# Kernel tuning notes

Measured on AMD Instinct MI355X. Metric: run time of the kernel, lower is better.

The kernel has to match this reference:

```python
import jax, jax.numpy as jnp
import numpy as np

N_CAR, N_LIGHT, N_STOP = 180000, 10000, 10000
N = N_CAR + N_LIGHT + N_STOP
E = 6_400_000

# LossConfig defaults
LAMBDA_RECON, LAMBDA_RULE, LAMBDA_ATTN, LAMBDA_REG = 1.0, 0.5, 0.3, 1e-4
W_ATTN_GAT, W_ATTN_RULE = 0.5, 0.5
VIOL_THRESH = 0.5


def setup_inputs() -> dict:
    key = jax.random.key(0)
    ks = jax.random.split(key, 8)
    eps = 1e-6
    model_scores = jnp.clip(jax.random.uniform(ks[0], (N_CAR,), jnp.float32), eps, 1.0 - eps)
    rule_scores = jnp.clip(jax.random.uniform(ks[1], (N_CAR,), jnp.float32), eps, 1.0 - eps)
    alpha_gat = jax.random.uniform(ks[2], (E,), jnp.float32)
    beta_rule = jax.random.uniform(ks[3], (N_CAR,), jnp.float32)
    src = jax.random.randint(ks[4], (E,), 0, N)
    dst = jax.random.randint(ks[5], (E,), 0, N)
    edge_index = jnp.stack([src, dst], axis=0)
    # cars first (type 0), then lights (1), then stop lines (2)
    entity_types = jnp.concatenate([
        jnp.zeros((N_CAR,), jnp.int32),
        jnp.ones((N_LIGHT,), jnp.int32),
        jnp.full((N_STOP,), 2, jnp.int32),
    ])
    param0 = jax.random.normal(ks[6], (4096, 4096), jnp.float32) * 0.02
    param1 = jax.random.normal(ks[7], (4096, 4096), jnp.float32) * 0.02
    return {
        "model_scores": model_scores, "rule_scores": rule_scores,
        "alpha_gat": alpha_gat, "beta_rule": beta_rule,
        "edge_index": edge_index, "entity_types": entity_types,
        "param0": param0, "param1": param1,
    }


def _bce(x, t):
    # torch F.binary_cross_entropy clamps log at -100
    log_x = jnp.clip(jnp.log(x), -100.0)
    log_1mx = jnp.clip(jnp.log1p(-x), -100.0)
    return jnp.mean(-(t * log_x + (1.0 - t) * log_1mx))


def _gat_attn_loss(alpha_gat, edge_index, entity_types, violation_mask):
    src, dst = edge_index[0], edge_index[1]
    dst_t = entity_types[dst]
    rule_edge = (dst_t == 1) | (dst_t == 2)
    masked = jnp.where(rule_edge, alpha_gat, -jnp.inf)
    # fused segment-max over source nodes replaces the per-car Python loop
    seg_max = jax.ops.segment_max(masked, src, num_segments=N)  # [N]
    car_ids = jnp.nonzero(entity_types == 0, size=N_CAR)[0]      # [N_car]
    max_attn = seg_max[car_ids]                                  # [N_car]
    valid = jnp.isfinite(max_attn) & violation_mask             # cars w/ rule neighbor
    safe = jnp.where(valid, max_attn, 0.0)
    total = jnp.sum(jnp.where(valid, (1.0 - safe) ** 2, 0.0))
    cnt = jnp.sum(valid)
    return jnp.where(cnt > 0, total / jnp.maximum(cnt, 1).astype(total.dtype), 0.0)


def _rule_attn_loss(beta_rule, violation_mask):
    total = jnp.sum(jnp.where(violation_mask, (1.0 - beta_rule) ** 2, 0.0))
    cnt = jnp.sum(violation_mask)
    return jnp.where(cnt > 0, total / jnp.maximum(cnt, 1).astype(total.dtype), 0.0)


@jax.jit
def reference(model_scores, rule_scores, alpha_gat, beta_rule, edge_index, entity_types, param0, param1):
    L_recon = _bce(model_scores, rule_scores)
    L_rule = jnp.mean((model_scores - rule_scores) ** 2)
    violation_mask = rule_scores > VIOL_THRESH
    any_viol = jnp.any(violation_mask)
    L_attn_gat = jnp.where(any_viol, _gat_attn_loss(alpha_gat, edge_index, entity_types, violation_mask), 0.0)
    L_attn_rule = jnp.where(any_viol, _rule_attn_loss(beta_rule, violation_mask), 0.0)
    L_attn = W_ATTN_GAT * L_attn_gat + W_ATTN_RULE * L_attn_rule
    L_reg = jnp.sum(param0 ** 2) + jnp.sum(param1 ** 2)
    L_total = (LAMBDA_RECON * L_recon + LAMBDA_RULE * L_rule
               + LAMBDA_ATTN * L_attn + LAMBDA_REG * L_reg)
    num_violations = jnp.sum(violation_mask).astype(jnp.float32)
    return (L_total, L_recon, L_rule, L_attn, L_attn_gat, L_attn_rule, L_reg, num_violations)
```

## Files before the change

kernel.cpp:

```cpp
#include <hip/hip_runtime.h>

#define N_CAR   180000
#define NE      6400000
#define P_ELEMS (4096 * 4096)
#define P4      (P_ELEMS / 4)

#define WORK_BLOCKS  4096
#define WORK_T       (WORK_BLOCKS * 256)
#define REG_ITERS    (P4 / WORK_T)
#define EDGE_QUADS   (NE / 4)

#define CAR_BLOCKS   ((N_CAR + 255) / 256)
#define MASK_WORDS   5632
#define MASK_QUADS   (MASK_WORDS / 4)
#define MASK_BLOCKS  704
#define NCOPY        8

typedef float    f4 __attribute__((ext_vector_type(4)));
typedef int      i4 __attribute__((ext_vector_type(4)));
typedef unsigned u32;


__device__ __forceinline__ float wave_reduce_sum(float s) {
#pragma unroll
    for (int off = 32; off > 0; off >>= 1) s += __shfl_down(s, off, 64);
    return s;
}

__global__ void __launch_bounds__(256) mask_kernel(const float* __restrict__ rs,
                                                   u32* __restrict__ mask) {
    int j = blockIdx.x * 256 + threadIdx.x;
    int bit = (j < N_CAR) && (rs[j] > 0.5f);
    unsigned long long b = __ballot(bit);
    if ((threadIdx.x & 63) == 0) {
        int w = (j >> 6) * 2;
        mask[w]     = (u32)(b);
        mask[w + 1] = (u32)(b >> 32);
    }
}

template <int NC, int SCOPE>
__global__ void __launch_bounds__(256) work_kernel(const i4* __restrict__ src4,
                                                   const i4* __restrict__ dst4,
                                                   const f4* __restrict__ alpha4,
                                                   int* __restrict__ segmax,
                                                   const u32* __restrict__ maskg,
                                                   const f4* __restrict__ p0,
                                                   const f4* __restrict__ p1,
                                                   float* __restrict__ regpart) {
    __shared__ u32 smask[MASK_WORDS];
    __shared__ float red[4];
    int t = blockIdx.x * 256 + threadIdx.x;

    {
        const i4* m4 = (const i4*)maskg;
        i4* s4 = (i4*)smask;
        for (int q = threadIdx.x; q < MASK_QUADS; q += 256) s4[q] = m4[q];
    }

    int base = 0;
    if (NC > 1) {
        int xcd = (int)(__builtin_amdgcn_s_getreg((31u << 11) | 20) & (NC - 1));
        base = xcd * N_CAR;
    }
    __syncthreads();

    for (int q = t; q < EDGE_QUADS; q += WORK_T) {
        i4 d  = __builtin_nontemporal_load(&dst4[q]);
        i4 sv = __builtin_nontemporal_load(&src4[q]);
        f4 al = __builtin_nontemporal_load(&alpha4[q]);
#define EDGE_DO(C)                                                              \
        if (d.C >= N_CAR && sv.C < N_CAR &&                                     \
            ((smask[sv.C >> 5] >> (sv.C & 31)) & 1u)) {                         \
            __hip_atomic_fetch_max(&segmax[base + sv.C], __float_as_int(al.C),  \
                                   __ATOMIC_RELAXED, SCOPE);                    \
        }
        EDGE_DO(x)
        EDGE_DO(y)
        EDGE_DO(z)
        EDGE_DO(w)
#undef EDGE_DO
    }

    f4 a = {0.f, 0.f, 0.f, 0.f};
#pragma unroll
    for (int k = 0; k < REG_ITERS; ++k) {
        f4 v = __builtin_nontemporal_load(&p0[t + k * WORK_T]);
        a += v * v;
    }
#pragma unroll
    for (int k = 0; k < REG_ITERS; ++k) {
        f4 v = __builtin_nontemporal_load(&p1[t + k * WORK_T]);
        a += v * v;
    }
    float s = (a.x + a.y) + (a.z + a.w);
    s = wave_reduce_sum(s);
    int wave = threadIdx.x >> 6;
    int lane = threadIdx.x & 63;
    if (lane == 0) red[wave] = s;
    __syncthreads();
    if (threadIdx.x == 0)
        regpart[blockIdx.x] = red[0] + red[1] + red[2] + red[3];
}

template <int NC>
__global__ void __launch_bounds__(256) car_kernel(const float* __restrict__ ms,
                                                  const float* __restrict__ rs,
                                                  const float* __restrict__ beta,
                                                  const int* __restrict__ segmax,
                                                  float* __restrict__ carpart) {
    int i = blockIdx.x * blockDim.x + threadIdx.x;
    float vals[6] = {0.f, 0.f, 0.f, 0.f, 0.f, 0.f};
    if (i < N_CAR) {
        float x = ms[i];
        float t = rs[i];
        float lx  = fmaxf(logf(x), -100.0f);
        float l1x = fmaxf(log1pf(-x), -100.0f);
        vals[0] = -(t * lx + (1.0f - t) * l1x);
        float df = x - t;
        vals[1] = df * df;
        if (t > 0.5f) {
            vals[2] = 1.0f;
            float b = beta[i];
            vals[3] = (1.0f - b) * (1.0f - b);
            int mi = segmax[i];
#pragma unroll
            for (int c = 1; c < NC; ++c)
                mi = max(mi, segmax[c * N_CAR + i]);
            if (mi >= 0) {
                float m = __int_as_float(mi);
                vals[4] = (1.0f - m) * (1.0f - m);
                vals[5] = 1.0f;
            }
        }
    }
    __shared__ float red[4][6];
    int wave = threadIdx.x >> 6;
    int lane = threadIdx.x & 63;
#pragma unroll
    for (int k = 0; k < 6; ++k) {
        float s = wave_reduce_sum(vals[k]);
        if (lane == 0) red[wave][k] = s;
    }
    __syncthreads();
    if (threadIdx.x == 0) {
#pragma unroll
        for (int k = 0; k < 6; ++k)
            carpart[blockIdx.x * 6 + k] = red[0][k] + red[1][k] + red[2][k] + red[3][k];
    }
}

__global__ void __launch_bounds__(256) finalize_kernel(const float* __restrict__ regpart,
                                                       const float* __restrict__ carpart,
                                                       float* __restrict__ out) {
    int tid = threadIdx.x;
    float rsum = 0.0f;
    for (int i = tid; i < WORK_BLOCKS; i += 256) rsum += regpart[i];
    float c[6] = {0.f, 0.f, 0.f, 0.f, 0.f, 0.f};
    for (int r = tid; r < CAR_BLOCKS; r += 256) {
#pragma unroll
        for (int k = 0; k < 6; ++k) c[k] += carpart[r * 6 + k];
    }
    __shared__ float red[4][7];
    int wave = tid >> 6;
    int lane = tid & 63;
    {
        float s = wave_reduce_sum(rsum);
        if (lane == 0) red[wave][6] = s;
    }
#pragma unroll
    for (int k = 0; k < 6; ++k) {
        float s = wave_reduce_sum(c[k]);
        if (lane == 0) red[wave][k] = s;
    }
    __syncthreads();
    if (tid == 0) {
        float tot[7];
#pragma unroll
        for (int k = 0; k < 7; ++k)
            tot[k] = red[0][k] + red[1][k] + red[2][k] + red[3][k];
        const float inv_ncar = 1.0f / (float)N_CAR;
        float L_recon = tot[0] * inv_ncar;
        float L_rule  = tot[1] * inv_ncar;
        float vc      = tot[2];
        float L_attn_rule = (vc > 0.0f) ? tot[3] / vc : 0.0f;
        float gat_cnt = tot[5];
        float L_attn_gat = (vc > 0.0f && gat_cnt > 0.0f) ? tot[4] / gat_cnt : 0.0f;
        float L_attn = 0.5f * L_attn_gat + 0.5f * L_attn_rule;
        float L_reg  = tot[6];
        float L_total = 1.0f * L_recon + 0.5f * L_rule + 0.3f * L_attn + 1e-4f * L_reg;
        out[0] = L_total;
        out[1] = L_recon;
        out[2] = L_rule;
        out[3] = L_attn;
        out[4] = L_attn_gat;
        out[5] = L_attn_rule;
        out[6] = L_reg;
        out[7] = vc;
    }
}

extern "C" void kernel_launch(void* const* d_in, const int* in_sizes, int n_in,
                              void* d_out, int out_size, void* d_ws, size_t ws_size,
                              hipStream_t stream) {
    const float* model_scores = (const float*)d_in[0];
    const float* rule_scores  = (const float*)d_in[1];
    const float* alpha_gat    = (const float*)d_in[2];
    const float* beta_rule    = (const float*)d_in[3];
    const int*   edge_index   = (const int*)d_in[4];
    const float* param0       = (const float*)d_in[6];
    const float* param1       = (const float*)d_in[7];
    float* out = (float*)d_out;

    const int* src = edge_index;
    const int* dst = edge_index + NE;

    const size_t seg_bytes8 = (size_t)NCOPY * N_CAR * sizeof(int);
    const size_t tail_bytes = (size_t)(MASK_WORDS + WORK_BLOCKS + CAR_BLOCKS * 6) * 4;

    if (ws_size >= seg_bytes8 + tail_bytes) {
        int* segmax  = (int*)d_ws;
        u32* mask    = (u32*)((char*)d_ws + seg_bytes8);
        float* regpart = (float*)(mask + MASK_WORDS);
        float* carpart = regpart + WORK_BLOCKS;

        mask_kernel<<<MASK_BLOCKS, 256, 0, stream>>>(rule_scores, mask);
        work_kernel<NCOPY, __HIP_MEMORY_SCOPE_WORKGROUP>
            <<<WORK_BLOCKS, 256, 0, stream>>>(
                (const i4*)src, (const i4*)dst, (const f4*)alpha_gat, segmax,
                mask, (const f4*)param0, (const f4*)param1, regpart);
        car_kernel<NCOPY><<<CAR_BLOCKS, 256, 0, stream>>>(
            model_scores, rule_scores, beta_rule, segmax, carpart);
        finalize_kernel<<<1, 256, 0, stream>>>(regpart, carpart, out);
    } else {
        int* segmax  = (int*)d_ws;
        u32* mask    = (u32*)((char*)d_ws + (size_t)N_CAR * sizeof(int));
        float* regpart = (float*)(mask + MASK_WORDS);
        float* carpart = regpart + WORK_BLOCKS;

        mask_kernel<<<MASK_BLOCKS, 256, 0, stream>>>(rule_scores, mask);
        work_kernel<1, __HIP_MEMORY_SCOPE_AGENT>
            <<<WORK_BLOCKS, 256, 0, stream>>>(
                (const i4*)src, (const i4*)dst, (const f4*)alpha_gat, segmax,
                mask, (const f4*)param0, (const f4*)param1, regpart);
        car_kernel<1><<<CAR_BLOCKS, 256, 0, stream>>>(
            model_scores, rule_scores, beta_rule, segmax, carpart);
        finalize_kernel<<<1, 256, 0, stream>>>(regpart, carpart, out);
    }
}
```

Baseline: 218.1 us.

## Drop violation-mask kernel and issue all edge and param loads upfront

Removes the separate mask kernel and the shared-memory violation-mask filter, so edges whose source is any car now perform the atomic max. The violation mask is presumably applied later in car_kernel. The edge loop is fully unrolled into two fixed quads per thread, and all parameter loads are issued before the atomics so memory latency overlaps. It also drops the nontemporal hints. In exchange, about twice as many atomics run, and the many live f4 registers may lower occupancy.

```diff
diff --git a/kernel.cpp b/kernel.cpp
--- a/kernel.cpp
+++ b/kernel.cpp
@@ -11,32 +11,16 @@
 #define EDGE_QUADS   (NE / 4)
 
 #define CAR_BLOCKS   ((N_CAR + 255) / 256)
-#define MASK_WORDS   5632
-#define MASK_QUADS   (MASK_WORDS / 4)
-#define MASK_BLOCKS  704
 #define NCOPY        8
 
 typedef float    f4 __attribute__((ext_vector_type(4)));
 typedef int      i4 __attribute__((ext_vector_type(4)));
-typedef unsigned u32;
 
 
 __device__ __forceinline__ float wave_reduce_sum(float s) {
 #pragma unroll
     for (int off = 32; off > 0; off >>= 1) s += __shfl_down(s, off, 64);
     return s;
-}
-
-__global__ void __launch_bounds__(256) mask_kernel(const float* __restrict__ rs,
-                                                   u32* __restrict__ mask) {
-    int j = blockIdx.x * 256 + threadIdx.x;
-    int bit = (j < N_CAR) && (rs[j] > 0.5f);
-    unsigned long long b = __ballot(bit);
-    if ((threadIdx.x & 63) == 0) {
-        int w = (j >> 6) * 2;
-        mask[w]     = (u32)(b);
-        mask[w + 1] = (u32)(b >> 32);
-    }
 }
 
 template <int NC, int SCOPE>
@@ -44,57 +28,53 @@
                                                    const i4* __restrict__ dst4,
                                                    const f4* __restrict__ alpha4,
                                                    int* __restrict__ segmax,
-                                                   const u32* __restrict__ maskg,
                                                    const f4* __restrict__ p0,
                                                    const f4* __restrict__ p1,
                                                    float* __restrict__ regpart) {
-    __shared__ u32 smask[MASK_WORDS];
-    __shared__ float red[4];
     int t = blockIdx.x * 256 + threadIdx.x;
-
-    {
-        const i4* m4 = (const i4*)maskg;
-        i4* s4 = (i4*)smask;
-        for (int q = threadIdx.x; q < MASK_QUADS; q += 256) s4[q] = m4[q];
-    }
 
     int base = 0;
     if (NC > 1) {
         int xcd = (int)(__builtin_amdgcn_s_getreg((31u << 11) | 20) & (NC - 1));
         base = xcd * N_CAR;
     }
-    __syncthreads();
-
-    for (int q = t; q < EDGE_QUADS; q += WORK_T) {
-        i4 d  = __builtin_nontemporal_load(&dst4[q]);
-        i4 sv = __builtin_nontemporal_load(&src4[q]);
-        f4 al = __builtin_nontemporal_load(&alpha4[q]);
-#define EDGE_DO(C)                                                              \
-        if (d.C >= N_CAR && sv.C < N_CAR &&                                     \
-            ((smask[sv.C >> 5] >> (sv.C & 31)) & 1u)) {                         \
-            __hip_atomic_fetch_max(&segmax[base + sv.C], __float_as_int(al.C),  \
-                                   __ATOMIC_RELAXED, SCOPE);                    \
-        }
-        EDGE_DO(x)
-        EDGE_DO(y)
-        EDGE_DO(z)
-        EDGE_DO(w)
+
+    const bool has2 = (t + WORK_T) < EDGE_QUADS;
+    const int  q1   = has2 ? (t + WORK_T) : t;
+    i4 d0 = dst4[t];
+    i4 s0 = src4[t];
+    f4 a0 = alpha4[t];
+    i4 d1 = dst4[q1];
+    i4 s1 = src4[q1];
+    f4 a1 = alpha4[q1];
+
+    f4 v[2 * REG_ITERS];
+#pragma unroll
+    for (int k = 0; k < REG_ITERS; ++k) v[k] = p0[t + k * WORK_T];
+#pragma unroll
+    for (int k = 0; k < REG_ITERS; ++k) v[REG_ITERS + k] = p1[t + k * WORK_T];
+
+#define EDGE_DO(d, sv, al, C, live)                                             \
+    if ((live) && (d).C >= N_CAR && (sv).C < N_CAR) {                           \
+        __hip_atomic_fetch_max(&segmax[base + (sv).C], __float_as_int((al).C),  \
+                               __ATOMIC_RELAXED, SCOPE);                        \
+    }
+    EDGE_DO(d0, s0, a0, x, true)
+    EDGE_DO(d0, s0, a0, y, true)
+    EDGE_DO(d0, s0, a0, z, true)
+    EDGE_DO(d0, s0, a0, w, true)
+    EDGE_DO(d1, s1, a1, x, has2)
+    EDGE_DO(d1, s1, a1, y, has2)
+    EDGE_DO(d1, s1, a1, z, has2)
+    EDGE_DO(d1, s1, a1, w, has2)
 #undef EDGE_DO
-    }
-
-    f4 a = {0.f, 0.f, 0.f, 0.f};
-#pragma unroll
-    for (int k = 0; k < REG_ITERS; ++k) {
-        f4 v = __builtin_nontemporal_load(&p0[t + k * WORK_T]);
-        a += v * v;
-    }
-#pragma unroll
-    for (int k = 0; k < REG_ITERS; ++k) {
-        f4 v = __builtin_nontemporal_load(&p1[t + k * WORK_T]);
-        a += v * v;
-    }
+
+    f4 a = v[0] * v[0];
+#pragma unroll
+    for (int k = 1; k < 2 * REG_ITERS; ++k) a += v[k] * v[k];
     float s = (a.x + a.y) + (a.z + a.w);
     s = wave_reduce_sum(s);
+    __shared__ float red[4];
     int wave = threadIdx.x >> 6;
     int lane = threadIdx.x & 63;
     if (lane == 0) red[wave] = s;
@@ -216,33 +196,29 @@
     const int* dst = edge_index + NE;
 
     const size_t seg_bytes8 = (size_t)NCOPY * N_CAR * sizeof(int);
-    const size_t tail_bytes = (size_t)(MASK_WORDS + WORK_BLOCKS + CAR_BLOCKS * 6) * 4;
+    const size_t tail_bytes = (size_t)(WORK_BLOCKS + CAR_BLOCKS * 6) * 4;
 
     if (ws_size >= seg_bytes8 + tail_bytes) {
         int* segmax  = (int*)d_ws;
-        u32* mask    = (u32*)((char*)d_ws + seg_bytes8);
-        float* regpart = (float*)(mask + MASK_WORDS);
+        float* regpart = (float*)((char*)d_ws + seg_bytes8);
         float* carpart = regpart + WORK_BLOCKS;
 
-        mask_kernel<<<MASK_BLOCKS, 256, 0, stream>>>(rule_scores, mask);
         work_kernel<NCOPY, __HIP_MEMORY_SCOPE_WORKGROUP>
             <<<WORK_BLOCKS, 256, 0, stream>>>(
                 (const i4*)src, (const i4*)dst, (const f4*)alpha_gat, segmax,
-                mask, (const f4*)param0, (const f4*)param1, regpart);
+                (const f4*)param0, (const f4*)param1, regpart);
         car_kernel<NCOPY><<<CAR_BLOCKS, 256, 0, stream>>>(
             model_scores, rule_scores, beta_rule, segmax, carpart);
         finalize_kernel<<<1, 256, 0, stream>>>(regpart, carpart, out);
     } else {
         int* segmax  = (int*)d_ws;
-        u32* mask    = (u32*)((char*)d_ws + (size_t)N_CAR * sizeof(int));
-        float* regpart = (float*)(mask + MASK_WORDS);
+        float* regpart = (float*)((char*)d_ws + (size_t)N_CAR * sizeof(int));
         float* carpart = regpart + WORK_BLOCKS;
 
-        mask_kernel<<<MASK_BLOCKS, 256, 0, stream>>>(rule_scores, mask);
         work_kernel<1, __HIP_MEMORY_SCOPE_AGENT>
             <<<WORK_BLOCKS, 256, 0, stream>>>(
                 (const i4*)src, (const i4*)dst, (const f4*)alpha_gat, segmax,
-                mask, (const f4*)param0, (const f4*)param1, regpart);
+                (const f4*)param0, (const f4*)param1, regpart);
         car_kernel<1><<<CAR_BLOCKS, 256, 0, stream>>>(
             model_scores, rule_scores, beta_rule, segmax, carpart);
         finalize_kernel<<<1, 256, 0, stream>>>(regpart, carpart, out);
```

New measurement: 232.9 us. 1.07x slower.
